# Kernel tuning notes

Hardware: AMD Instinct MI355X
Metric: run time of the kernel (lower is better)

The kernel has to match this reference:

```python
import jax, jax.numpy as jnp
import numpy as np

D_MODEL = 1024
NUM_HEADS = 16
HEAD_DIM = D_MODEL // NUM_HEADS
NEG_INF = -1e9


def setup_inputs() -> dict:
    key = jax.random.key(0)
    ks = jax.random.split(key, 9)
    B, S, SI = 4, 1024, 512
    scale = 1.0 / np.sqrt(D_MODEL)
    return {
        "hidden_states": jax.random.normal(ks[0], (B, S, D_MODEL), jnp.float32),
        "image_hidden_states": jax.random.normal(ks[1], (B, SI, D_MODEL), jnp.float32),
        "attention_mask": jax.random.randint(ks[2], (B, 1, S, S + SI), 0, 2, jnp.int32),
        "w_q": jax.random.normal(ks[3], (D_MODEL, D_MODEL), jnp.float32) * scale,
        "w_k": jax.random.normal(ks[4], (D_MODEL, D_MODEL), jnp.float32) * scale,
        "w_v": jax.random.normal(ks[5], (D_MODEL, D_MODEL), jnp.float32) * scale,
        "u_k": jax.random.normal(ks[6], (D_MODEL, D_MODEL), jnp.float32) * scale,
        "u_v": jax.random.normal(ks[7], (D_MODEL, D_MODEL), jnp.float32) * scale,
        "w_o": jax.random.normal(ks[8], (D_MODEL, D_MODEL), jnp.float32) * scale,
    }


def _split_heads(x):
    # [B, S, D] -> [B, H, S, Dh]
    B, S, _ = x.shape
    return x.reshape(B, S, NUM_HEADS, HEAD_DIM).transpose(0, 2, 1, 3)


def reference(hidden_states, image_hidden_states, attention_mask,
              w_q, w_k, w_v, u_k, u_v, w_o):
    # nn.Linear(bias=False): y = x @ W.T
    q = _split_heads(hidden_states @ w_q.T)          # [B,H,S,Dh]
    k = _split_heads(hidden_states @ w_k.T)          # [B,H,S,Dh]
    v = _split_heads(hidden_states @ w_v.T)
    k_img = _split_heads(image_hidden_states @ u_k.T)  # [B,H,SI,Dh]
    v_img = _split_heads(image_hidden_states @ u_v.T)
    k = jnp.concatenate([k, k_img], axis=2)          # [B,H,S+SI,Dh]
    v = jnp.concatenate([v, v_img], axis=2)

    scores = jnp.einsum('bhqd,bhkd->bhqk', q, k) / np.sqrt(HEAD_DIM)
    scores = jnp.where(attention_mask == 0, NEG_INF, scores)
    p_attn = jax.nn.softmax(scores, axis=-1)         # dropout p=0.0 (eval)
    x = jnp.einsum('bhqk,bhkd->bhqd', p_attn, v)     # [B,H,S,Dh]
    B, H, S, Dh = x.shape
    x = x.transpose(0, 2, 1, 3).reshape(B, S, D_MODEL)
    return x @ w_o.T
```

## Files before the change

kernel.cpp:

```cpp
#include <hip/hip_runtime.h>
#include <stdint.h>


typedef unsigned short u16;
typedef short bf16x8v __attribute__((ext_vector_type(8)));
typedef float f32x4 __attribute__((ext_vector_type(4)));

__device__ __forceinline__ u16 f2bf(float f) {
  union { float f; uint32_t u; } x; x.f = f;
  uint32_t r = x.u + 0x7FFFu + ((x.u >> 16) & 1u);
  return (u16)(r >> 16);
}

__device__ __forceinline__ uint32_t cvtpk(float a, float b) {
  uint32_t r;
  asm("v_cvt_pk_bf16_f32 %0, %1, %2" : "=v"(r) : "v"(a), "v"(b));
  return r;
}

__device__ __forceinline__ float maskand(float e, uint32_t msrc, int off) {
  uint32_t mm = (uint32_t)((int32_t)(msrc << (31 - off)) >> 31);
  union { float f; uint32_t u; } x; x.f = e; x.u &= mm; return x.f;
}

__device__ __forceinline__ void gl_lds16(const u16* g, u16* l) {
  __builtin_amdgcn_global_load_lds((const __attribute__((address_space(1))) unsigned int*)g,
                                   (__attribute__((address_space(3))) unsigned int*)l,
                                   16, 0, 0);
}

__global__ __launch_bounds__(512, 2) void gemm_qkv(
    const float* __restrict__ Hs, const float* __restrict__ Im,
    const float* __restrict__ Wq, const float* __restrict__ Wk, const float* __restrict__ Wv,
    const float* __restrict__ Uk, const float* __restrict__ Uv,
    const int* __restrict__ Mk,
    u16* __restrict__ Qd, u16* __restrict__ Kd, u16* __restrict__ Vd,
    uint32_t* __restrict__ Mw)
{
  __shared__ __align__(16) u16 As[2 * 16384];
  __shared__ __align__(16) u16 Bs[2 * 16384];
  const int hb = blockIdx.x;
  const int xcd = hb & 7, slot = hb >> 3;
  int bid = (slot < 24) ? xcd * 24 + slot : 192 + xcd * 8 + (slot - 24);
  const float *Ap, *Bp;
  int bm, bn, mode;
  if (bid < 192) { mode = 4; bm = (bid / 12) * 256; bn = (bid % 12) * 256;
                   Ap = Hs + (size_t)bm * 1024;
                   Bp = ((bn < 1024) ? Wq : (bn < 2048) ? Wk : Wv) + (size_t)(bn & 1023) * 1024; }
  else           { mode = 5; int r = bid - 192; bm = (r >> 3) * 256; bn = (r & 7) * 256;
                   Ap = Im + (size_t)bm * 1024;
                   Bp = ((bn < 1024) ? Uk : Uv) + (size_t)(bn & 1023) * 1024; }
  const int tid = threadIdx.x, lane = tid & 63, wave = tid >> 6;
  const int wr = wave >> 2, wc = wave & 3;
  const int g = lane >> 4, c = lane & 15, cs = c & 7;
  const int srow = tid >> 3;
  const int pch  = tid & 7;
  const int gsw  = (pch ^ (srow & 7)) * 8;

  f32x4 zf = {0.f, 0.f, 0.f, 0.f};
  f32x4 acc[8][4];
  #pragma unroll
  for (int f = 0; f < 8; ++f)
    #pragma unroll
    for (int nf = 0; nf < 4; ++nf) acc[f][nf] = zf;

  float4 sa[4][2], sb[4][2];

  #define LOAD_A(kt)                                                               \
    _Pragma("unroll")                                                              \
    for (int j_ = 0; j_ < 4; ++j_) {                                               \
      const float* p_ = Ap + (size_t)(j_ * 64 + srow) * 1024 + (kt) * 64 + gsw;    \
      sa[j_][0] = *(const float4*)p_;                                              \
      sa[j_][1] = *(const float4*)(p_ + 4);                                        \
    }
  #define LOAD_B(kt)                                                               \
    _Pragma("unroll")                                                              \
    for (int j_ = 0; j_ < 4; ++j_) {                                               \
      const float* p_ = Bp + (size_t)(j_ * 64 + srow) * 1024 + (kt) * 64 + gsw;    \
      sb[j_][0] = *(const float4*)p_;                                              \
      sb[j_][1] = *(const float4*)(p_ + 4);                                        \
    }
  #define CVT_A(buf)                                                               \
    _Pragma("unroll")                                                              \
    for (int j_ = 0; j_ < 4; ++j_) {                                               \
      uint4 w_;                                                                    \
      w_.x = cvtpk(sa[j_][0].x, sa[j_][0].y);                                      \
      w_.y = cvtpk(sa[j_][0].z, sa[j_][0].w);                                      \
      w_.z = cvtpk(sa[j_][1].x, sa[j_][1].y);                                      \
      w_.w = cvtpk(sa[j_][1].z, sa[j_][1].w);                                      \
      *(uint4*)&As[(buf) + (j_ * 64 + srow) * 64 + pch * 8] = w_;                  \
    }
  #define CVT_B(buf)                                                               \
    _Pragma("unroll")                                                              \
    for (int j_ = 0; j_ < 4; ++j_) {                                               \
      uint4 w_;                                                                    \
      w_.x = cvtpk(sb[j_][0].x, sb[j_][0].y);                                      \
      w_.y = cvtpk(sb[j_][0].z, sb[j_][0].w);                                      \
      w_.z = cvtpk(sb[j_][1].x, sb[j_][1].y);                                      \
      w_.w = cvtpk(sb[j_][1].z, sb[j_][1].w);                                      \
      *(uint4*)&Bs[(buf) + (j_ * 64 + srow) * 64 + pch * 8] = w_;                  \
    }

  LOAD_A(0); LOAD_B(0);
  {
    const int fid = hb * 512 + tid;
    #pragma unroll 1
    for (int w = fid; w < 196608; w += 131072) {
      const int4* p = (const int4*)(Mk + (size_t)w * 32);
      uint32_t bits = 0;
      #pragma unroll 1
      for (int h_ = 0; h_ < 2; ++h_) {
        int4 v0 = p[h_ * 4 + 0], v1 = p[h_ * 4 + 1];
        int4 v2 = p[h_ * 4 + 2], v3 = p[h_ * 4 + 3];
        int bo = h_ * 16;
        bits |= (uint32_t)(v0.x != 0) << (bo + 0);
        bits |= (uint32_t)(v0.y != 0) << (bo + 1);
        bits |= (uint32_t)(v0.z != 0) << (bo + 2);
        bits |= (uint32_t)(v0.w != 0) << (bo + 3);
        bits |= (uint32_t)(v1.x != 0) << (bo + 4);
        bits |= (uint32_t)(v1.y != 0) << (bo + 5);
        bits |= (uint32_t)(v1.z != 0) << (bo + 6);
        bits |= (uint32_t)(v1.w != 0) << (bo + 7);
        bits |= (uint32_t)(v2.x != 0) << (bo + 8);
        bits |= (uint32_t)(v2.y != 0) << (bo + 9);
        bits |= (uint32_t)(v2.z != 0) << (bo + 10);
        bits |= (uint32_t)(v2.w != 0) << (bo + 11);
        bits |= (uint32_t)(v3.x != 0) << (bo + 12);
        bits |= (uint32_t)(v3.y != 0) << (bo + 13);
        bits |= (uint32_t)(v3.z != 0) << (bo + 14);
        bits |= (uint32_t)(v3.w != 0) << (bo + 15);
      }
      Mw[w] = bits;
    }
  }
  CVT_A(0);  CVT_B(0);
  __syncthreads();

  for (int kt = 0; kt < 16; ++kt) {
    const int bc = (kt & 1) * 16384;
    const int bx = bc ^ 16384;
    if (kt < 15) { LOAD_A(kt + 1); LOAD_B(kt + 1); }

    bf16x8v Bf[4][2];
    #pragma unroll
    for (int nf = 0; nf < 4; ++nf)
      #pragma unroll
      for (int ks = 0; ks < 2; ++ks)
        Bf[nf][ks] = *(const bf16x8v*)&Bs[bc + (wc * 64 + nf * 16 + c) * 64 + ((ks * 4 + g) ^ cs) * 8];

    #pragma unroll
    for (int p = 0; p < 4; ++p) {
      bf16x8v Af[2][2];
      #pragma unroll
      for (int i = 0; i < 2; ++i)
        #pragma unroll
        for (int ks = 0; ks < 2; ++ks)
          Af[i][ks] = *(const bf16x8v*)&As[bc + (wr * 128 + (p * 2 + i) * 16 + c) * 64 + ((ks * 4 + g) ^ cs) * 8];
      __builtin_amdgcn_s_setprio(1);
      #pragma unroll
      for (int i = 0; i < 2; ++i)
        #pragma unroll
        for (int nf = 0; nf < 4; ++nf)
          #pragma unroll
          for (int ks = 0; ks < 2; ++ks)
            acc[p * 2 + i][nf] =
              __builtin_amdgcn_mfma_f32_16x16x32_bf16(Af[i][ks], Bf[nf][ks], acc[p * 2 + i][nf], 0, 0, 0);
      __builtin_amdgcn_s_setprio(0);
      if (p == 1 && kt < 15) {
        __builtin_amdgcn_sched_barrier(0);
        CVT_A(bx);
        __builtin_amdgcn_sched_barrier(0);
      }
    }
    if (kt < 15) {
      __builtin_amdgcn_sched_barrier(0);
      CVT_B(bx);
    }
    __syncthreads();
  }
  #undef LOAD_A
  #undef LOAD_B
  #undef CVT_A
  #undef CVT_B

  const int gn0 = bn + wc * 64;
  if (mode == 4) {
    if (bn < 1024) {
      #pragma unroll
      for (int f = 0; f < 8; ++f)
        #pragma unroll
        for (int nf = 0; nf < 4; ++nf) {
          int gm = bm + wr * 128 + f * 16 + 4 * g;
          int gn = gn0 + nf * 16 + c;
          #pragma unroll
          for (int j = 0; j < 4; ++j)
            Qd[(size_t)(gm + j) * 1024 + gn] = f2bf(acc[f][nf][j] * 0.18033688011112042f);
        }
    } else if (bn < 2048) {
      #pragma unroll
      for (int f = 0; f < 8; ++f)
        #pragma unroll
        for (int nf = 0; nf < 4; ++nf) {
          int gm = bm + wr * 128 + f * 16 + 4 * g;
          int b_ = gm >> 10, s_ = gm & 1023;
          int gn = gn0 - 1024 + nf * 16 + c;
          #pragma unroll
          for (int j = 0; j < 4; ++j)
            Kd[(size_t)(b_ * 1536 + s_ + j) * 1024 + gn] = f2bf(acc[f][nf][j]);
        }
    } else {
      #pragma unroll
      for (int f = 0; f < 8; ++f)
        #pragma unroll
        for (int nf = 0; nf < 4; ++nf) {
          int gm = bm + wr * 128 + f * 16 + 4 * g;
          int b_ = gm >> 10, s_ = gm & 1023;
          int d_ = gn0 - 2048 + nf * 16 + c;
          uint2 st;
          st.x = cvtpk(acc[f][nf][0], acc[f][nf][1]);
          st.y = cvtpk(acc[f][nf][2], acc[f][nf][3]);
          *(uint2*)&Vd[(size_t)(b_ * 1024 + d_) * 1536 + s_] = st;
        }
    }
  } else {
    if (bn < 1024) {
      #pragma unroll
      for (int f = 0; f < 8; ++f)
        #pragma unroll
        for (int nf = 0; nf < 4; ++nf) {
          int gm = bm + wr * 128 + f * 16 + 4 * g;
          int b_ = gm >> 9, s_ = gm & 511;
          int gn = gn0 + nf * 16 + c;
          #pragma unroll
          for (int j = 0; j < 4; ++j)
            Kd[(size_t)(b_ * 1536 + 1024 + s_ + j) * 1024 + gn] = f2bf(acc[f][nf][j]);
        }
    } else {
      #pragma unroll
      for (int f = 0; f < 8; ++f)
        #pragma unroll
        for (int nf = 0; nf < 4; ++nf) {
          int gm = bm + wr * 128 + f * 16 + 4 * g;
          int b_ = gm >> 9, s_ = gm & 511;
          int d_ = gn0 - 1024 + nf * 16 + c;
          uint2 st;
          st.x = cvtpk(acc[f][nf][0], acc[f][nf][1]);
          st.y = cvtpk(acc[f][nf][2], acc[f][nf][3]);
          *(uint2*)&Vd[(size_t)(b_ * 1024 + d_) * 1536 + 1024 + s_] = st;
        }
    }
  }
}

__global__ __launch_bounds__(256) void gemm_out(const u16* __restrict__ A, const float* __restrict__ Bw,
                                                float* __restrict__ Cout)
{
  __shared__ __align__(16) u16 As2[2 * 8192];
  __shared__ __align__(16) u16 Bs2[2 * 8192];
  const int hb = blockIdx.x;
  const int xcd = hb & 7, slot = hb >> 3;
  const int rg = xcd * 4 + (slot >> 3);
  const int cg = slot & 7;
  const int bm = rg * 128, bn = cg * 128;
  const int tid  = threadIdx.x;
  const int lane = tid & 63, wave = tid >> 6;
  const int wr = wave >> 1, wc = wave & 1;
  const int g = lane >> 4, c = lane & 15, cs = c & 7;
  const int sr  = tid >> 3;
  const int pch = tid & 7;
  const int gsw = (pch ^ (sr & 7)) * 8;

  f32x4 zf = {0.f, 0.f, 0.f, 0.f};
  f32x4 acc[4][4];
  #pragma unroll
  for (int mi = 0; mi < 4; ++mi)
    #pragma unroll
    for (int ni = 0; ni < 4; ++ni) acc[mi][ni] = zf;

  float4 sb[4][2];

  #define STG_A(buf, kt)                                                           \
    _Pragma("unroll")                                                              \
    for (int q_ = 0; q_ < 4; ++q_) {                                               \
      int row_ = q_ * 32 + sr;                                                     \
      gl_lds16(A + (size_t)(bm + row_) * 1024 + (kt) * 64 + gsw,                   \
               &As2[(buf) + row_ * 64 + pch * 8]);                                 \
    }
  #define LOAD_B(kt)                                                               \
    _Pragma("unroll")                                                              \
    for (int q_ = 0; q_ < 4; ++q_) {                                               \
      const float* p_ = Bw + (size_t)(bn + q_ * 32 + sr) * 1024 + (kt) * 64 + gsw; \
      sb[q_][0] = *(const float4*)p_;                                              \
      sb[q_][1] = *(const float4*)(p_ + 4);                                        \
    }
  #define CVT_B(buf)                                                               \
    _Pragma("unroll")                                                              \
    for (int q_ = 0; q_ < 4; ++q_) {                                               \
      uint4 w_;                                                                    \
      w_.x = cvtpk(sb[q_][0].x, sb[q_][0].y);                                      \
      w_.y = cvtpk(sb[q_][0].z, sb[q_][0].w);                                      \
      w_.z = cvtpk(sb[q_][1].x, sb[q_][1].y);                                      \
      w_.w = cvtpk(sb[q_][1].z, sb[q_][1].w);                                      \
      *(uint4*)&Bs2[(buf) + (q_ * 32 + sr) * 64 + pch * 8] = w_;                   \
    }

  STG_A(0, 0);
  LOAD_B(0);
  CVT_B(0);
  __syncthreads();

  for (int kt = 0; kt < 16; ++kt) {
    const int bc = (kt & 1) * 8192;
    const int bx = bc ^ 8192;
    if (kt < 15) { STG_A(bx, kt + 1); LOAD_B(kt + 1); }

    #pragma unroll
    for (int ks = 0; ks < 2; ++ks) {
      bf16x8v af[4], bfr[4];
      #pragma unroll
      for (int mi = 0; mi < 4; ++mi)
        af[mi] = *(const bf16x8v*)&As2[bc + (wr * 64 + mi * 16 + c) * 64 + ((ks * 4 + g) ^ cs) * 8];
      #pragma unroll
      for (int ni = 0; ni < 4; ++ni)
        bfr[ni] = *(const bf16x8v*)&Bs2[bc + (wc * 64 + ni * 16 + c) * 64 + ((ks * 4 + g) ^ cs) * 8];
      __builtin_amdgcn_s_setprio(1);
      #pragma unroll
      for (int mi = 0; mi < 4; ++mi)
        #pragma unroll
        for (int ni = 0; ni < 4; ++ni)
          acc[mi][ni] = __builtin_amdgcn_mfma_f32_16x16x32_bf16(af[mi], bfr[ni], acc[mi][ni], 0, 0, 0);
      __builtin_amdgcn_s_setprio(0);
    }
    if (kt < 15) {
      __builtin_amdgcn_sched_barrier(0);
      CVT_B(bx);
    }
    __syncthreads();
  }
  #undef STG_A
  #undef LOAD_B
  #undef CVT_B

  #pragma unroll
  for (int mi = 0; mi < 4; ++mi)
    #pragma unroll
    for (int ni = 0; ni < 4; ++ni)
      #pragma unroll
      for (int j = 0; j < 4; ++j) {
        int gm = bm + wr * 64 + mi * 16 + 4 * g + j;
        int gn = bn + wc * 64 + ni * 16 + c;
        Cout[(size_t)gm * 1024 + gn] = acc[mi][ni][j];
      }
}

__global__ __launch_bounds__(256) void attn_kernel(const u16* __restrict__ Q, const u16* __restrict__ Kc,
                                                   const u16* __restrict__ Vt,
                                                   const uint32_t* __restrict__ Mw,
                                                   u16* __restrict__ AO)
{
  const int bid = blockIdx.x;
  const int grp = bid & 63;
  const int qt  = bid >> 6;
  const int h = grp & 15, b = grp >> 4;
  const int q0 = qt * 64;
  const int tid = threadIdx.x, lane = tid & 63, wave = tid >> 6;
  const int g = lane >> 4, c = lane & 15;
  const int qw = q0 + wave * 16;

  __shared__ __align__(16) u16 Ks[64 * 64];
  __shared__ __align__(16) u16 Vs[64 * 64];
  __shared__ __align__(16) u16 Ps[4][16 * 72];

  bf16x8v qf0, qf1;
  {
    const u16* qp = Q + (size_t)(b * 1024 + qw + c) * 1024 + h * 64 + g * 8;
    qf0 = *(const bf16x8v*)qp;
    qf1 = *(const bf16x8v*)(qp + 32);
  }
  f32x4 zf = {0.f, 0.f, 0.f, 0.f};
  f32x4 O[4];
  float l = 0.f;
  #pragma unroll
  for (int dt = 0; dt < 4; ++dt) O[dt] = zf;

  const int sr  = tid >> 3;
  const int pch = tid & 7;
  const int swz = (pch ^ (sr & 7)) * 8;
  const int cs  = c & 7;
  const u16* Kbase = Kc + (size_t)(b * 1536) * 1024 + h * 64;
  const u16* Vbase = Vt + (size_t)(b * 1024 + h * 64) * 1536;
  const uint32_t* mrow = Mw + (size_t)(b * 1024 + qw + c) * 48;

  bf16x8v kr0, kr1, vr0, vr1;
  kr0 = *(const bf16x8v*)(Kbase + (size_t)sr * 1024 + pch * 8);
  kr1 = *(const bf16x8v*)(Kbase + (size_t)(32 + sr) * 1024 + pch * 8);
  vr0 = *(const bf16x8v*)(Vbase + (size_t)sr * 1536 + pch * 8);
  vr1 = *(const bf16x8v*)(Vbase + (size_t)(32 + sr) * 1536 + pch * 8);
  *(bf16x8v*)&Ks[sr * 64 + swz]        = kr0;
  *(bf16x8v*)&Ks[(32 + sr) * 64 + swz] = kr1;
  *(bf16x8v*)&Vs[sr * 64 + swz]        = vr0;
  *(bf16x8v*)&Vs[(32 + sr) * 64 + swz] = vr1;
  __syncthreads();

  for (int kt = 0; kt < 24; ++kt) {
    if (kt < 23) {
      const int ln = (kt + 1) * 64;
      kr0 = *(const bf16x8v*)(Kbase + (size_t)(ln + sr) * 1024 + pch * 8);
      kr1 = *(const bf16x8v*)(Kbase + (size_t)(ln + 32 + sr) * 1024 + pch * 8);
      vr0 = *(const bf16x8v*)(Vbase + (size_t)sr * 1536 + ln + pch * 8);
      vr1 = *(const bf16x8v*)(Vbase + (size_t)(32 + sr) * 1536 + ln + pch * 8);
    }
    uint2 mwv = *(const uint2*)(mrow + kt * 2);

    f32x4 s[4];
    __builtin_amdgcn_s_setprio(1);
    #pragma unroll
    for (int nt = 0; nt < 4; ++nt) {
      const u16* kr = &Ks[(nt * 16 + c) * 64];
      bf16x8v k0 = *(const bf16x8v*)&kr[(g ^ cs) * 8];
      bf16x8v k1 = *(const bf16x8v*)&kr[((4 + g) ^ cs) * 8];
      f32x4 z = zf;
      z = __builtin_amdgcn_mfma_f32_16x16x32_bf16(k0, qf0, z, 0, 0, 0);
      z = __builtin_amdgcn_mfma_f32_16x16x32_bf16(k1, qf1, z, 0, 0, 0);
      s[nt] = z;
    }
    __builtin_amdgcn_s_setprio(0);

    uint64_t mq = (((uint64_t)mwv.y << 32) | (uint64_t)mwv.x) >> (4 * g);
    uint32_t mlo = (uint32_t)mq, mhi = (uint32_t)(mq >> 32);
    #pragma unroll
    for (int nt = 0; nt < 4; ++nt) {
      uint32_t msrc = (nt < 2) ? mlo : mhi;
      #pragma unroll
      for (int j = 0; j < 4; ++j) {
        float e = exp2f(s[nt][j]);
        float p = maskand(e, msrc, 16 * (nt & 1) + j);
        s[nt][j] = p;
        l += p;
      }
    }

    u16* pw = &Ps[wave][0];
    #pragma unroll
    for (int nt = 0; nt < 4; ++nt) {
      uint2 pk2;
      pk2.x = cvtpk(s[nt][0], s[nt][1]);
      pk2.y = cvtpk(s[nt][2], s[nt][3]);
      *(uint2*)&pw[c * 72 + nt * 16 + g * 4] = pk2;
    }
    bf16x8v pb0 = *(const bf16x8v*)&pw[c * 72 + g * 8];
    bf16x8v pb1 = *(const bf16x8v*)&pw[c * 72 + 32 + g * 8];
    __builtin_amdgcn_s_setprio(1);
    #pragma unroll
    for (int dt = 0; dt < 4; ++dt) {
      const u16* vr = &Vs[(dt * 16 + c) * 64];
      bf16x8v v0 = *(const bf16x8v*)&vr[(g ^ cs) * 8];
      bf16x8v v1 = *(const bf16x8v*)&vr[((4 + g) ^ cs) * 8];
      O[dt] = __builtin_amdgcn_mfma_f32_16x16x32_bf16(v0, pb0, O[dt], 0, 0, 0);
      O[dt] = __builtin_amdgcn_mfma_f32_16x16x32_bf16(v1, pb1, O[dt], 0, 0, 0);
    }
    __builtin_amdgcn_s_setprio(0);

    __syncthreads();
    if (kt < 23) {
      *(bf16x8v*)&Ks[sr * 64 + swz]        = kr0;
      *(bf16x8v*)&Ks[(32 + sr) * 64 + swz] = kr1;
      *(bf16x8v*)&Vs[sr * 64 + swz]        = vr0;
      *(bf16x8v*)&Vs[(32 + sr) * 64 + swz] = vr1;
      __syncthreads();
    }
  }

  float r = l;
  r += __shfl_xor(r, 16);
  r += __shfl_xor(r, 32);
  float inv = 1.f / r;
  size_t ro = (size_t)(b * 1024 + qw + c) * 1024 + h * 64;
  #pragma unroll
  for (int dt = 0; dt < 4; ++dt) {
    uint2 st;
    st.x = cvtpk(O[dt][0] * inv, O[dt][1] * inv);
    st.y = cvtpk(O[dt][2] * inv, O[dt][3] * inv);
    *(uint2*)&AO[ro + dt * 16 + 4 * g] = st;
  }
}

extern "C" void kernel_launch(void* const* d_in, const int* in_sizes, int n_in,
                              void* d_out, int out_size, void* d_ws, size_t ws_size,
                              hipStream_t stream) {
  (void)in_sizes; (void)n_in; (void)out_size; (void)ws_size;
  const float* hs = (const float*)d_in[0];
  const float* im = (const float*)d_in[1];
  const int*   mk = (const int*)d_in[2];
  const float* wq = (const float*)d_in[3];
  const float* wk = (const float*)d_in[4];
  const float* wv = (const float*)d_in[5];
  const float* uk = (const float*)d_in[6];
  const float* uv = (const float*)d_in[7];
  const float* wo = (const float*)d_in[8];

  char* ws = (char*)d_ws;
  u16* Qb  = (u16*)(ws + 0);
  u16* Kb  = (u16*)(ws + 8388608);
  u16* Vtb = (u16*)(ws + 20971520);
  u16* AO  = (u16*)(ws + 33554432);
  uint32_t* Mw = (uint32_t*)(ws + 41943040);

  gemm_qkv<<<256, 512, 0, stream>>>(hs, im, wq, wk, wv, uk, uv, mk, Qb, Kb, Vtb, Mw);
  attn_kernel<<<1024, 256, 0, stream>>>(Qb, Kb, Vtb, Mw, AO);
  gemm_out<<<256, 256, 0, stream>>>(AO, wo, (float*)d_out);
}
```

Before: 137.1 us.

## Single-buffer QKV GEMM LDS and double query rows per attention wave

The QKV projection GEMM drops its double-buffered LDS staging for a single buffer and raises the launch-bounds occupancy hint to 4, adding an extra barrier per k-step instead of overlapping conversion with MFMA. The attention kernel now has each wave process 32 query rows instead of 16, so each K/V tile loaded into LDS is reused for twice as many queries, and the grid is halved to 512 blocks. The intent is to cut K/V reload traffic in attention and raise occupancy in the GEMM. The cost is higher register pressure in attention, fewer blocks, and less latency hiding in the GEMM.

```diff
diff --git a/kernel.cpp b/kernel.cpp
--- a/kernel.cpp
+++ b/kernel.cpp
@@ -29,7 +29,7 @@
                                    16, 0, 0);
 }
 
-__global__ __launch_bounds__(512, 2) void gemm_qkv(
+__global__ __launch_bounds__(512, 4) void gemm_qkv(
     const float* __restrict__ Hs, const float* __restrict__ Im,
     const float* __restrict__ Wq, const float* __restrict__ Wk, const float* __restrict__ Wv,
     const float* __restrict__ Uk, const float* __restrict__ Uv,
@@ -37,8 +37,8 @@
     u16* __restrict__ Qd, u16* __restrict__ Kd, u16* __restrict__ Vd,
     uint32_t* __restrict__ Mw)
 {
-  __shared__ __align__(16) u16 As[2 * 16384];
-  __shared__ __align__(16) u16 Bs[2 * 16384];
+  __shared__ __align__(16) u16 As[16384];
+  __shared__ __align__(16) u16 Bs[16384];
   const int hb = blockIdx.x;
   const int xcd = hb & 7, slot = hb >> 3;
   int bid = (slot < 24) ? xcd * 24 + slot : 192 + xcd * 8 + (slot - 24);
@@ -80,7 +80,7 @@
       sb[j_][0] = *(const float4*)p_;                                              \
       sb[j_][1] = *(const float4*)(p_ + 4);                                        \
     }
-  #define CVT_A(buf)                                                               \
+  #define CVT_A()                                                                  \
     _Pragma("unroll")                                                              \
     for (int j_ = 0; j_ < 4; ++j_) {                                               \
       uint4 w_;                                                                    \
@@ -88,9 +88,9 @@
       w_.y = cvtpk(sa[j_][0].z, sa[j_][0].w);                                      \
       w_.z = cvtpk(sa[j_][1].x, sa[j_][1].y);                                      \
       w_.w = cvtpk(sa[j_][1].z, sa[j_][1].w);                                      \
-      *(uint4*)&As[(buf) + (j_ * 64 + srow) * 64 + pch * 8] = w_;                  \
-    }
-  #define CVT_B(buf)                                                               \
+      *(uint4*)&As[(j_ * 64 + srow) * 64 + pch * 8] = w_;                          \
+    }
+  #define CVT_B()                                                                  \
     _Pragma("unroll")                                                              \
     for (int j_ = 0; j_ < 4; ++j_) {                                               \
       uint4 w_;                                                                    \
@@ -98,7 +98,7 @@
       w_.y = cvtpk(sb[j_][0].z, sb[j_][0].w);                                      \
       w_.z = cvtpk(sb[j_][1].x, sb[j_][1].y);                                      \
       w_.w = cvtpk(sb[j_][1].z, sb[j_][1].w);                                      \
-      *(uint4*)&Bs[(buf) + (j_ * 64 + srow) * 64 + pch * 8] = w_;                  \
+      *(uint4*)&Bs[(j_ * 64 + srow) * 64 + pch * 8] = w_;                          \
     }
 
   LOAD_A(0); LOAD_B(0);
@@ -133,12 +133,10 @@
       Mw[w] = bits;
     }
   }
-  CVT_A(0);  CVT_B(0);
+  CVT_A(); CVT_B();
   __syncthreads();
 
   for (int kt = 0; kt < 16; ++kt) {
-    const int bc = (kt & 1) * 16384;
-    const int bx = bc ^ 16384;
     if (kt < 15) { LOAD_A(kt + 1); LOAD_B(kt + 1); }
 
     bf16x8v Bf[4][2];
@@ -146,7 +144,7 @@
     for (int nf = 0; nf < 4; ++nf)
       #pragma unroll
       for (int ks = 0; ks < 2; ++ks)
-        Bf[nf][ks] = *(const bf16x8v*)&Bs[bc + (wc * 64 + nf * 16 + c) * 64 + ((ks * 4 + g) ^ cs) * 8];
+        Bf[nf][ks] = *(const bf16x8v*)&Bs[(wc * 64 + nf * 16 + c) * 64 + ((ks * 4 + g) ^ cs) * 8];
 
     #pragma unroll
     for (int p = 0; p < 4; ++p) {
@@ -155,7 +153,7 @@
       for (int i = 0; i < 2; ++i)
         #pragma unroll
         for (int ks = 0; ks < 2; ++ks)
-          Af[i][ks] = *(const bf16x8v*)&As[bc + (wr * 128 + (p * 2 + i) * 16 + c) * 64 + ((ks * 4 + g) ^ cs) * 8];
+          Af[i][ks] = *(const bf16x8v*)&As[(wr * 128 + (p * 2 + i) * 16 + c) * 64 + ((ks * 4 + g) ^ cs) * 8];
       __builtin_amdgcn_s_setprio(1);
       #pragma unroll
       for (int i = 0; i < 2; ++i)
@@ -166,17 +164,12 @@
             acc[p * 2 + i][nf] =
               __builtin_amdgcn_mfma_f32_16x16x32_bf16(Af[i][ks], Bf[nf][ks], acc[p * 2 + i][nf], 0, 0, 0);
       __builtin_amdgcn_s_setprio(0);
-      if (p == 1 && kt < 15) {
-        __builtin_amdgcn_sched_barrier(0);
-        CVT_A(bx);
-        __builtin_amdgcn_sched_barrier(0);
-      }
-    }
+    }
+    __syncthreads();
     if (kt < 15) {
-      __builtin_amdgcn_sched_barrier(0);
-      CVT_B(bx);
-    }
-    __syncthreads();
+      CVT_A(); CVT_B();
+      __syncthreads();
+    }
   }
   #undef LOAD_A
   #undef LOAD_B
@@ -362,26 +355,28 @@
   const int grp = bid & 63;
   const int qt  = bid >> 6;
   const int h = grp & 15, b = grp >> 4;
-  const int q0 = qt * 64;
+  const int q0 = qt * 128;
   const int tid = threadIdx.x, lane = tid & 63, wave = tid >> 6;
   const int g = lane >> 4, c = lane & 15;
-  const int qw = q0 + wave * 16;
+  const int qw = q0 + wave * 32;
 
   __shared__ __align__(16) u16 Ks[64 * 64];
   __shared__ __align__(16) u16 Vs[64 * 64];
-  __shared__ __align__(16) u16 Ps[4][16 * 72];
-
-  bf16x8v qf0, qf1;
+  __shared__ __align__(16) u16 Ps[4][32 * 72];
+
+  bf16x8v qf00, qf01, qf10, qf11;
   {
     const u16* qp = Q + (size_t)(b * 1024 + qw + c) * 1024 + h * 64 + g * 8;
-    qf0 = *(const bf16x8v*)qp;
-    qf1 = *(const bf16x8v*)(qp + 32);
+    qf00 = *(const bf16x8v*)qp;
+    qf01 = *(const bf16x8v*)(qp + 32);
+    qf10 = *(const bf16x8v*)(qp + 16 * 1024);
+    qf11 = *(const bf16x8v*)(qp + 16 * 1024 + 32);
   }
   f32x4 zf = {0.f, 0.f, 0.f, 0.f};
-  f32x4 O[4];
-  float l = 0.f;
+  f32x4 O0[4], O1[4];
+  float l0 = 0.f, l1 = 0.f;
   #pragma unroll
-  for (int dt = 0; dt < 4; ++dt) O[dt] = zf;
+  for (int dt = 0; dt < 4; ++dt) { O0[dt] = zf; O1[dt] = zf; }
 
   const int sr  = tid >> 3;
   const int pch = tid & 7;
@@ -389,7 +384,8 @@
   const int cs  = c & 7;
   const u16* Kbase = Kc + (size_t)(b * 1536) * 1024 + h * 64;
   const u16* Vbase = Vt + (size_t)(b * 1024 + h * 64) * 1536;
-  const uint32_t* mrow = Mw + (size_t)(b * 1024 + qw + c) * 48;
+  const uint32_t* mrow0 = Mw + (size_t)(b * 1024 + qw + c) * 48;
+  const uint32_t* mrow1 = mrow0 + 16 * 48;
 
   bf16x8v kr0, kr1, vr0, vr1;
   kr0 = *(const bf16x8v*)(Kbase + (size_t)sr * 1024 + pch * 8);
@@ -410,33 +406,53 @@
       vr0 = *(const bf16x8v*)(Vbase + (size_t)sr * 1536 + ln + pch * 8);
       vr1 = *(const bf16x8v*)(Vbase + (size_t)(32 + sr) * 1536 + ln + pch * 8);
     }
-    uint2 mwv = *(const uint2*)(mrow + kt * 2);
-
-    f32x4 s[4];
+    uint2 mwv0 = *(const uint2*)(mrow0 + kt * 2);
+    uint2 mwv1 = *(const uint2*)(mrow1 + kt * 2);
+
+    f32x4 s0[4], s1[4];
     __builtin_amdgcn_s_setprio(1);
     #pragma unroll
     for (int nt = 0; nt < 4; ++nt) {
       const u16* kr = &Ks[(nt * 16 + c) * 64];
       bf16x8v k0 = *(const bf16x8v*)&kr[(g ^ cs) * 8];
       bf16x8v k1 = *(const bf16x8v*)&kr[((4 + g) ^ cs) * 8];
-      f32x4 z = zf;
-      z = __builtin_amdgcn_mfma_f32_16x16x32_bf16(k0, qf0, z, 0, 0, 0);
-      z = __builtin_amdgcn_mfma_f32_16x16x32_bf16(k1, qf1, z, 0, 0, 0);
-      s[nt] = z;
+      f32x4 z0 = zf, z1 = zf;
+      z0 = __builtin_amdgcn_mfma_f32_16x16x32_bf16(k0, qf00, z0, 0, 0, 0);
+      z0 = __builtin_amdgcn_mfma_f32_16x16x32_bf16(k1, qf01, z0, 0, 0, 0);
+      z1 = __builtin_amdgcn_mfma_f32_16x16x32_bf16(k0, qf10, z1, 0, 0, 0);
+      z1 = __builtin_amdgcn_mfma_f32_16x16x32_bf16(k1, qf11, z1, 0, 0, 0);
+      s0[nt] = z0; s1[nt] = z1;
     }
     __builtin_amdgcn_s_setprio(0);
 
-    uint64_t mq = (((uint64_t)mwv.y << 32) | (uint64_t)mwv.x) >> (4 * g);
-    uint32_t mlo = (uint32_t)mq, mhi = (uint32_t)(mq >> 32);
-    #pragma unroll
-    for (int nt = 0; nt < 4; ++nt) {
-      uint32_t msrc = (nt < 2) ? mlo : mhi;
-      #pragma unroll
-      for (int j = 0; j < 4; ++j) {
-        float e = exp2f(s[nt][j]);
-        float p = maskand(e, msrc, 16 * (nt & 1) + j);
-        s[nt][j] = p;
-        l += p;
+    {
+      uint64_t mq = (((uint64_t)mwv0.y << 32) | (uint64_t)mwv0.x) >> (4 * g);
+      uint32_t mlo = (uint32_t)mq, mhi = (uint32_t)(mq >> 32);
+      #pragma unroll
+      for (int nt = 0; nt < 4; ++nt) {
+        uint32_t msrc = (nt < 2) ? mlo : mhi;
+        #pragma unroll
+        for (int j = 0; j < 4; ++j) {
+          float e = exp2f(s0[nt][j]);
+          float p = maskand(e, msrc, 16 * (nt & 1) + j);
+          s0[nt][j] = p;
+          l0 += p;
+        }
+      }
+    }
+    {
+      uint64_t mq = (((uint64_t)mwv1.y << 32) | (uint64_t)mwv1.x) >> (4 * g);
+      uint32_t mlo = (uint32_t)mq, mhi = (uint32_t)(mq >> 32);
+      #pragma unroll
+      for (int nt = 0; nt < 4; ++nt) {
+        uint32_t msrc = (nt < 2) ? mlo : mhi;
+        #pragma unroll
+        for (int j = 0; j < 4; ++j) {
+          float e = exp2f(s1[nt][j]);
+          float p = maskand(e, msrc, 16 * (nt & 1) + j);
+          s1[nt][j] = p;
+          l1 += p;
+        }
       }
     }
 
@@ -444,20 +460,27 @@
     #pragma unroll
     for (int nt = 0; nt < 4; ++nt) {
       uint2 pk2;
-      pk2.x = cvtpk(s[nt][0], s[nt][1]);
-      pk2.y = cvtpk(s[nt][2], s[nt][3]);
+      pk2.x = cvtpk(s0[nt][0], s0[nt][1]);
+      pk2.y = cvtpk(s0[nt][2], s0[nt][3]);
       *(uint2*)&pw[c * 72 + nt * 16 + g * 4] = pk2;
-    }
-    bf16x8v pb0 = *(const bf16x8v*)&pw[c * 72 + g * 8];
-    bf16x8v pb1 = *(const bf16x8v*)&pw[c * 72 + 32 + g * 8];
+      pk2.x = cvtpk(s1[nt][0], s1[nt][1]);
+      pk2.y = cvtpk(s1[nt][2], s1[nt][3]);
+      *(uint2*)&pw[(16 + c) * 72 + nt * 16 + g * 4] = pk2;
+    }
+    bf16x8v pb00 = *(const bf16x8v*)&pw[c * 72 + g * 8];
+    bf16x8v pb01 = *(const bf16x8v*)&pw[c * 72 + 32 + g * 8];
+    bf16x8v pb10 = *(const bf16x8v*)&pw[(16 + c) * 72 + g * 8];
+    bf16x8v pb11 = *(const bf16x8v*)&pw[(16 + c) * 72 + 32 + g * 8];
     __builtin_amdgcn_s_setprio(1);
     #pragma unroll
     for (int dt = 0; dt < 4; ++dt) {
       const u16* vr = &Vs[(dt * 16 + c) * 64];
       bf16x8v v0 = *(const bf16x8v*)&vr[(g ^ cs) * 8];
       bf16x8v v1 = *(const bf16x8v*)&vr[((4 + g) ^ cs) * 8];
-      O[dt] = __builtin_amdgcn_mfma_f32_16x16x32_bf16(v0, pb0, O[dt], 0, 0, 0);
-      O[dt] = __builtin_amdgcn_mfma_f32_16x16x32_bf16(v1, pb1, O[dt], 0, 0, 0);
+      O0[dt] = __builtin_amdgcn_mfma_f32_16x16x32_bf16(v0, pb00, O0[dt], 0, 0, 0);
+      O0[dt] = __builtin_amdgcn_mfma_f32_16x16x32_bf16(v1, pb01, O0[dt], 0, 0, 0);
+      O1[dt] = __builtin_amdgcn_mfma_f32_16x16x32_bf16(v0, pb10, O1[dt], 0, 0, 0);
+      O1[dt] = __builtin_amdgcn_mfma_f32_16x16x32_bf16(v1, pb11, O1[dt], 0, 0, 0);
     }
     __builtin_amdgcn_s_setprio(0);
 
@@ -471,17 +494,25 @@
     }
   }
 
-  float r = l;
-  r += __shfl_xor(r, 16);
-  r += __shfl_xor(r, 32);
-  float inv = 1.f / r;
-  size_t ro = (size_t)(b * 1024 + qw + c) * 1024 + h * 64;
+  float r0 = l0;
+  r0 += __shfl_xor(r0, 16);
+  r0 += __shfl_xor(r0, 32);
+  float inv0 = 1.f / r0;
+  float r1 = l1;
+  r1 += __shfl_xor(r1, 16);
+  r1 += __shfl_xor(r1, 32);
+  float inv1 = 1.f / r1;
+  size_t ro0 = (size_t)(b * 1024 + qw + c) * 1024 + h * 64;
+  size_t ro1 = ro0 + (size_t)16 * 1024;
   #pragma unroll
   for (int dt = 0; dt < 4; ++dt) {
     uint2 st;
-    st.x = cvtpk(O[dt][0] * inv, O[dt][1] * inv);
-    st.y = cvtpk(O[dt][2] * inv, O[dt][3] * inv);
-    *(uint2*)&AO[ro + dt * 16 + 4 * g] = st;
+    st.x = cvtpk(O0[dt][0] * inv0, O0[dt][1] * inv0);
+    st.y = cvtpk(O0[dt][2] * inv0, O0[dt][3] * inv0);
+    *(uint2*)&AO[ro0 + dt * 16 + 4 * g] = st;
+    st.x = cvtpk(O1[dt][0] * inv1, O1[dt][1] * inv1);
+    st.y = cvtpk(O1[dt][2] * inv1, O1[dt][3] * inv1);
+    *(uint2*)&AO[ro1 + dt * 16 + 4 * g] = st;
   }
 }
 
@@ -507,6 +538,6 @@
   uint32_t* Mw = (uint32_t*)(ws + 41943040);
 
   gemm_qkv<<<256, 512, 0, stream>>>(hs, im, wq, wk, wv, uk, uv, mk, Qb, Kb, Vtb, Mw);
-  attn_kernel<<<1024, 256, 0, stream>>>(Qb, Kb, Vtb, Mw, AO);
+  attn_kernel<<<512, 256, 0, stream>>>(Qb, Kb, Vtb, Mw, AO);
   gemm_out<<<256, 256, 0, stream>>>(AO, wo, (float*)d_out);
 }
```

Result: slower. 464.2 us (+238.6%).
